# Kernel tuning notes

Measured on AMD Instinct MI355X. Metric: run time of the kernel, lower is better.

## Reference

```python
import jax, jax.numpy as jnp
import numpy as np

EPS = 1e-8

def setup_inputs() -> dict:
    key = jax.random.key(0)
    k1, k2, k3 = jax.random.split(key, 3)
    B, N, M = 4, 8192, 8192
    source = jax.random.normal(k1, (B, N, 3), dtype=jnp.float32)
    target = jax.random.normal(k2, (B, M, 3), dtype=jnp.float32)
    weights = jax.random.uniform(k3, (B, N), dtype=jnp.float32)
    return {"source": source, "target": target, "weights": weights}

def reference(source, target, weights):
    # Pairwise squared distances: (B, N, M)
    diff = source[:, :, None, :] - target[:, None, :, :]
    sq_distances = jnp.sum(diff * diff, axis=-1)
    # squared=False -> take sqrt with eps for stability
    distances = jnp.sqrt(sq_distances + EPS)
    # source -> target nearest-neighbor distance, weighted
    s2t = jnp.min(distances, axis=2) * weights  # (B, N)
    forward_loss = jnp.mean(s2t)
    # symmetric=True: target -> source (unweighted, as in original)
    t2s = jnp.min(distances, axis=1)  # (B, M)
    backward_loss = jnp.mean(t2s)
    return forward_loss + backward_loss
```

## Files before the change

### kernel.cpp

```cpp
#include <hip/hip_runtime.h>
#include <math.h>


#define EPS 1e-8f

typedef _Float16 f16x8 __attribute__((ext_vector_type(8)));
typedef float    f32x16 __attribute__((ext_vector_type(16)));

constexpr int B_    = 4;
constexpr int N_    = 8192;
constexpr int TPB   = 256;
constexpr int QPW   = 64;
constexpr int QPB   = 4 * QPW;
constexpr int RCH   = 8;
constexpr int CHUNK = N_ / RCH;
constexpr int RB    = 64;

__global__ __launch_bounds__(TPB, 6)
void nn_mfma_kernel(const float* __restrict__ src, const float* __restrict__ tgt,
                    float* __restrict__ part, float* __restrict__ out)
{
    __shared__ f16x8 sref[CHUNK + 64];

    if (blockIdx.x == 0 && blockIdx.y == 0 && blockIdx.z == 0 && threadIdx.x == 0)
        out[0] = 0.f;

    const int zb  = blockIdx.z;
    const int dir = zb >> 2;
    const int b   = zb & 3;
    const float* Rraw = (dir ? src : tgt) + ((size_t)b * N_ + (size_t)blockIdx.y * CHUNK) * 3;
    const float* Qraw = (dir ? tgt : src) + (size_t)b * N_ * 3;
    float* opart = part + ((size_t)zb * RCH + blockIdx.y) * N_;

    const int tid = threadIdx.x;
    const _Float16 h0 = (_Float16)0.f;
    const _Float16 h1 = (_Float16)1.f;

    for (int k = tid; k < CHUNK; k += TPB) {
        const float* rp = Rraw + (size_t)k * 3;
        _Float16 hx = (_Float16)rp[0], hy = (_Float16)rp[1], hz = (_Float16)rp[2];
        float fx = (float)hx, fy = (float)hy, fz = (float)hz;
        float rsq = fx * fx + fy * fy + fz * fz;
        _Float16 rh = (_Float16)rsq;
        _Float16 rl = (_Float16)(rsq - (float)rh);
        f16x8 a = {(_Float16)(-2.f * fx), (_Float16)(-2.f * fy),
                   (_Float16)(-2.f * fz), rh, rl, h0, h0, h0};
        sref[k] = a;
    }
    if (tid < 64) {
        f16x8 z = {h0, h0, h0, h0, h0, h0, h0, h0};
        sref[CHUNK + tid] = z;
    }

    const int lane = tid & 63;
    const int wv   = tid >> 6;
    const int l31  = lane & 31;
    const int half = lane >> 5;
    const int qb   = blockIdx.x * QPB + wv * QPW;

    f16x8 B0 = {h0, h0, h0, h0, h0, h0, h0, h0};
    f16x8 B1 = B0;
    float qs0 = 0.f, qs1 = 0.f;
    if (half == 0) {
        const float* q0 = Qraw + (size_t)(qb + l31) * 3;
        const float* q1 = Qraw + (size_t)(qb + 32 + l31) * 3;
        _Float16 ax = (_Float16)q0[0], ay = (_Float16)q0[1], az = (_Float16)q0[2];
        _Float16 bx = (_Float16)q1[0], by = (_Float16)q1[1], bz = (_Float16)q1[2];
        float fax = (float)ax, fay = (float)ay, faz = (float)az;
        float fbx = (float)bx, fby = (float)by, fbz = (float)bz;
        B0 = f16x8{ax, ay, az, h1, h1, h0, h0, h0};
        B1 = f16x8{bx, by, bz, h1, h1, h0, h0, h0};
        qs0 = fax * fax + fay * fay + faz * faz;
        qs1 = fbx * fbx + fby * fby + fbz * fbz;
    }
    __syncthreads();

    const f32x16 zc = {};

    int idx = (half == 0) ? l31 : CHUNK;
    const int step = (half == 0) ? 32 : 0;
    float mn0a = 3.0e38f, mn0b = 3.0e38f, mn1a = 3.0e38f, mn1b = 3.0e38f;

    f16x8 a = sref[idx];
    idx += step;
    for (int s = 0; s < CHUNK / 32; ++s) {
        f16x8 an = sref[idx];
        idx += step;
        f32x16 d0 = __builtin_amdgcn_mfma_f32_32x32x16_f16(a, B0, zc, 0, 0, 0);
        f32x16 d1 = __builtin_amdgcn_mfma_f32_32x32x16_f16(a, B1, zc, 0, 0, 0);
#pragma unroll
        for (int r = 0; r < 8; r += 2)
            mn0a = fminf(fminf(d0[r], d0[r + 1]), mn0a);
#pragma unroll
        for (int r = 8; r < 16; r += 2)
            mn0b = fminf(fminf(d0[r], d0[r + 1]), mn0b);
#pragma unroll
        for (int r = 0; r < 8; r += 2)
            mn1a = fminf(fminf(d1[r], d1[r + 1]), mn1a);
#pragma unroll
        for (int r = 8; r < 16; r += 2)
            mn1b = fminf(fminf(d1[r], d1[r + 1]), mn1b);
        a = an;
    }

    float mn0 = fminf(mn0a, mn0b);
    float mn1 = fminf(mn1a, mn1b);
    mn0 = fminf(mn0, __shfl_xor(mn0, 32));
    mn1 = fminf(mn1, __shfl_xor(mn1, 32));
    if (half == 0) {
        opart[qb + l31]      = fmaxf(mn0 + qs0, 0.f);
        opart[qb + 32 + l31] = fmaxf(mn1 + qs1, 0.f);
    }
}

__global__ __launch_bounds__(TPB)
void reduce_kernel(const float* __restrict__ part,
                   const float* __restrict__ w,
                   float* __restrict__ out)
{
    const int Q = 2 * B_ * N_;
    const float invBN = 1.0f / (float)(B_ * N_);

    float sum = 0.0f;
    for (int t = blockIdx.x * TPB + threadIdx.x; t < Q; t += RB * TPB) {
        const int zb = t >> 13;
        const int qn = t & (N_ - 1);
        const float* p = part + ((size_t)zb * RCH) * N_ + qn;
        float m = p[0];
#pragma unroll
        for (int c = 1; c < RCH; ++c) m = fminf(m, p[(size_t)c * N_]);
        float d = sqrtf(m + EPS);
        sum += (zb < 4) ? d * w[(size_t)zb * N_ + qn] : d;
    }
    sum *= invBN;

    __shared__ float ss[TPB / 64];
    int lane = threadIdx.x & 63;
    int wid  = threadIdx.x >> 6;
#pragma unroll
    for (int off = 32; off > 0; off >>= 1) sum += __shfl_down(sum, off);
    if (lane == 0) ss[wid] = sum;
    __syncthreads();
    if (threadIdx.x == 0) {
        float s = 0.0f;
#pragma unroll
        for (int i = 0; i < TPB / 64; ++i) s += ss[i];
        atomicAdd(out, s);
    }
}

extern "C" void kernel_launch(void* const* d_in, const int* in_sizes, int n_in,
                              void* d_out, int out_size, void* d_ws, size_t ws_size,
                              hipStream_t stream)
{
    const float* src = (const float*)d_in[0];
    const float* tgt = (const float*)d_in[1];
    const float* w   = (const float*)d_in[2];
    float* out = (float*)d_out;

    float* part = (float*)d_ws;

    dim3 grid(N_ / QPB, RCH, 2 * B_);
    nn_mfma_kernel<<<grid, TPB, 0, stream>>>(src, tgt, part, out);

    reduce_kernel<<<RB, TPB, 0, stream>>>(part, w, out);
}
```

Measured before the change: 76.04 us.

## Software-pipeline MFMA with min-reduction using double-buffered accumulators

Restructures the inner loop so the MFMA for the next reference tile is issued before the min-fold of the previous tile's results. Two sets of accumulator registers alternate, which lets matrix-core latency overlap with VALU fminf work. Launch bounds drop from 6 to 4 waves per SIMD to leave room for the extra registers, at the cost of lower occupancy.

```diff
diff --git a/kernel.cpp b/kernel.cpp
--- a/kernel.cpp
+++ b/kernel.cpp
@@ -16,7 +16,15 @@
 constexpr int CHUNK = N_ / RCH;
 constexpr int RB    = 64;
 
-__global__ __launch_bounds__(TPB, 6)
+#define FOLD(d, ma, mb)                                         \
+    _Pragma("unroll")                                           \
+    for (int r = 0; r < 8; r += 2)                              \
+        ma = fminf(fminf(d[r], d[r + 1]), ma);                  \
+    _Pragma("unroll")                                           \
+    for (int r = 8; r < 16; r += 2)                             \
+        mb = fminf(fminf(d[r], d[r + 1]), mb);
+
+__global__ __launch_bounds__(TPB, 4)
 void nn_mfma_kernel(const float* __restrict__ src, const float* __restrict__ tgt,
                     float* __restrict__ part, float* __restrict__ out)
 {
@@ -83,24 +91,31 @@
 
     f16x8 a = sref[idx];
     idx += step;
-    for (int s = 0; s < CHUNK / 32; ++s) {
-        f16x8 an = sref[idx];
+    f32x16 dA0 = __builtin_amdgcn_mfma_f32_32x32x16_f16(a, B0, zc, 0, 0, 0);
+    f32x16 dA1 = __builtin_amdgcn_mfma_f32_32x32x16_f16(a, B1, zc, 0, 0, 0);
+    a = sref[idx];
+    idx += step;
+    for (int s = 0; s < 15; ++s) {
+        f32x16 dB0 = __builtin_amdgcn_mfma_f32_32x32x16_f16(a, B0, zc, 0, 0, 0);
+        f32x16 dB1 = __builtin_amdgcn_mfma_f32_32x32x16_f16(a, B1, zc, 0, 0, 0);
+        a = sref[idx];
         idx += step;
-        f32x16 d0 = __builtin_amdgcn_mfma_f32_32x32x16_f16(a, B0, zc, 0, 0, 0);
-        f32x16 d1 = __builtin_amdgcn_mfma_f32_32x32x16_f16(a, B1, zc, 0, 0, 0);
-#pragma unroll
-        for (int r = 0; r < 8; r += 2)
-            mn0a = fminf(fminf(d0[r], d0[r + 1]), mn0a);
-#pragma unroll
-        for (int r = 8; r < 16; r += 2)
-            mn0b = fminf(fminf(d0[r], d0[r + 1]), mn0b);
-#pragma unroll
-        for (int r = 0; r < 8; r += 2)
-            mn1a = fminf(fminf(d1[r], d1[r + 1]), mn1a);
-#pragma unroll
-        for (int r = 8; r < 16; r += 2)
-            mn1b = fminf(fminf(d1[r], d1[r + 1]), mn1b);
-        a = an;
+        FOLD(dA0, mn0a, mn0b)
+        FOLD(dA1, mn1a, mn1b)
+        dA0 = __builtin_amdgcn_mfma_f32_32x32x16_f16(a, B0, zc, 0, 0, 0);
+        dA1 = __builtin_amdgcn_mfma_f32_32x32x16_f16(a, B1, zc, 0, 0, 0);
+        a = sref[idx];
+        idx += step;
+        FOLD(dB0, mn0a, mn0b)
+        FOLD(dB1, mn1a, mn1b)
+    }
+    {
+        f32x16 dB0 = __builtin_amdgcn_mfma_f32_32x32x16_f16(a, B0, zc, 0, 0, 0);
+        f32x16 dB1 = __builtin_amdgcn_mfma_f32_32x32x16_f16(a, B1, zc, 0, 0, 0);
+        FOLD(dA0, mn0a, mn0b)
+        FOLD(dA1, mn1a, mn1b)
+        FOLD(dB0, mn0a, mn0b)
+        FOLD(dB1, mn1a, mn1b)
     }
 
     float mn0 = fminf(mn0a, mn0b);
```

After: 75.89 us. No clear change (-0.2%).
